# Kernel optimization log

Measured on AMD Instinct MI355X. Metric: run time of the kernel, lower is better.

## Reference

```python
import jax, jax.numpy as jnp
import numpy as np
import math

EPS = 1e-12


def _cmul(ar, ai, br, bi):
    return ar * br - ai * bi, ar * bi + ai * br


def _wilson_seed(x):
    # x: (B, 4, L, L) -> conj of canonical Wilson-line path, (B, L, L) re/im
    ux_r, ux_i, uy_r, uy_i = x[:, 0], x[:, 1], x[:, 2], x[:, 3]
    B, L, _ = ux_r.shape
    dt = x.dtype

    def step(c, u):
        cr, ci = c
        ur, ui = u
        nr, ni = _cmul(cr, ci, ur, ui)
        return (nr, ni), (nr, ni)

    # cumulative complex product along x at y=0
    init_r = jnp.ones((B,), dt)
    init_i = jnp.zeros((B,), dt)
    xs = (ux_r[:, :-1, 0].T, ux_i[:, :-1, 0].T)  # (L-1, B)
    _, (axr, axi) = jax.lax.scan(step, (init_r, init_i), xs)
    x_axis_r = jnp.concatenate([init_r[None], axr], 0).T  # (B, L)
    x_axis_i = jnp.concatenate([init_i[None], axi], 0).T

    # cumulative complex product along y, vectorized over x
    ys = (jnp.moveaxis(uy_r[:, :, :-1], 2, 0), jnp.moveaxis(uy_i[:, :, :-1], 2, 0))  # (L-1, B, L)
    _, (pr, pi_) = jax.lax.scan(step, (x_axis_r, x_axis_i), ys)
    path_r = jnp.moveaxis(jnp.concatenate([x_axis_r[None], pr], 0), 0, 2)  # (B, L, L)
    path_i = jnp.moveaxis(jnp.concatenate([x_axis_i[None], pi_], 0), 0, 2)
    return path_r, -path_i  # conjugate


def _wrap(t):
    return (t + math.pi) % (2.0 * math.pi) - math.pi


def _initial_features(x):
    seed_r, seed_i = _wilson_seed(x)
    ax = jnp.arctan2(x[:, 1], x[:, 0])
    ay = jnp.arctan2(x[:, 3], x[:, 2])
    plaq = _wrap(ax + jnp.roll(ay, -1, axis=1) - jnp.roll(ax, -1, axis=2) - ay)
    pc = jnp.cos(plaq)
    pavg = (pc + jnp.roll(pc, 1, 1) + jnp.roll(pc, -1, 1)
            + jnp.roll(pc, 1, 2) + jnp.roll(pc, -1, 2)) / 5.0
    scalars = jnp.stack([jnp.ones_like(pc), pc, pavg], axis=1)  # (B, 3, L, L)
    return seed_r[:, None] * scalars, seed_i[:, None] * scalars


def _transport_fwd(fr, fi, x, mu):
    lr, li = (x[:, 0], x[:, 1]) if mu == 0 else (x[:, 2], x[:, 3])
    sr = jnp.roll(fr, -1, axis=mu + 2)
    si = jnp.roll(fi, -1, axis=mu + 2)
    return _cmul(lr[:, None], li[:, None], sr, si)


def _transport_bwd(fr, fi, x, mu):
    lr, li = (x[:, 0], x[:, 1]) if mu == 0 else (x[:, 2], x[:, 3])
    cr = jnp.roll(lr, 1, axis=mu + 1)
    ci = jnp.roll(-li, 1, axis=mu + 1)
    sr = jnp.roll(fr, 1, axis=mu + 2)
    si = jnp.roll(fi, 1, axis=mu + 2)
    return _cmul(cr[:, None], ci[:, None], sr, si)


def _lconv(fr, fi, x, center, fwd_w, bwd_w):
    out_r = jnp.einsum('oi,bixy->boxy', center, fr)
    out_i = jnp.einsum('oi,bixy->boxy', center, fi)
    for mu in range(2):
        fr2, fi2 = _transport_fwd(fr, fi, x, mu)
        br2, bi2 = _transport_bwd(fr, fi, x, mu)
        out_r = out_r + jnp.einsum('oi,bixy->boxy', fwd_w[mu], fr2) \
                      + jnp.einsum('oi,bixy->boxy', bwd_w[mu], br2)
        out_i = out_i + jnp.einsum('oi,bixy->boxy', fwd_w[mu], fi2) \
                      + jnp.einsum('oi,bixy->boxy', bwd_w[mu], bi2)
    return out_r, out_i


def _modrelu(fr, fi, bias):
    mag = jnp.sqrt(fr * fr + fi * fi + EPS)
    act = jax.nn.relu(mag + bias[None, :, None, None])
    scale = act / jnp.maximum(mag, EPS)
    return fr * scale, fi * scale


def setup_inputs() -> dict:
    key = jax.random.key(0)
    ks = jax.random.split(key, 11)
    B, L, H, O = 64, 128, 16, 8
    s = 0.1
    return {
        'x': jax.random.normal(ks[0], (B, 4, L, L), jnp.float32),
        'center1': s * jax.random.normal(ks[1], (H, 3), jnp.float32),
        'fwd_w1': s * jax.random.normal(ks[2], (2, H, 3), jnp.float32),
        'bwd_w1': s * jax.random.normal(ks[3], (2, H, 3), jnp.float32),
        'bias1': jnp.zeros((H,), jnp.float32),
        'center2': s * jax.random.normal(ks[4], (O, H), jnp.float32),
        'fwd_w2': s * jax.random.normal(ks[5], (2, O, H), jnp.float32),
        'bwd_w2': s * jax.random.normal(ks[6], (2, O, H), jnp.float32),
        'bias2': jnp.zeros((O,), jnp.float32),
        'ro_weight': s * jax.random.normal(ks[7], (O,), jnp.float32),
        'ro_bias': jnp.zeros((1,), jnp.float32),
    }


def reference(x, center1, fwd_w1, bwd_w1, bias1, center2, fwd_w2, bwd_w2, bias2, ro_weight, ro_bias):
    fr, fi = _initial_features(x)
    fr, fi = _lconv(fr, fi, x, center1, fwd_w1, bwd_w1)
    fr, fi = _modrelu(fr, fi, bias1)
    fr, fi = _lconv(fr, fi, x, center2, fwd_w2, bwd_w2)
    fr, fi = _modrelu(fr, fi, bias2)
    inv = fr * fr + fi * fi
    return jnp.einsum('c,bcxy->bxy', ro_weight, inv)[:, None] + ro_bias.reshape(1, 1, 1, 1)
```

## Files before the change

kernel.cpp:

```cpp
#include <hip/hip_runtime.h>
#include <math.h>

#define LQ   128
#define BQ   64
#define LL   (LQ*LQ)
#define H1   16
#define O2   8
#define TILE 16
#define REG  18
#define NPTS (REG*REG)
#define PCR  22
#define PCN  (PCR*PCR)
#define LKR  23
#define LKN  (LKR*LKR)
#define SDR  20
#define SDN  (SDR*SDR)
#define FSTR 10

typedef float f2 __attribute__((ext_vector_type(2)));
using bf8 = __attribute__((ext_vector_type(8))) short;
using f4  = __attribute__((ext_vector_type(4))) float;

__device__ __forceinline__ int wrapi(int v) { return v & (LQ - 1); }

__device__ __forceinline__ unsigned pack_bf(float hi, float lo) {
    return __builtin_amdgcn_perm(__float_as_uint(hi), __float_as_uint(lo),
                                 0x07060302u);
}
__device__ __forceinline__ unsigned bfrne(float f) {
    unsigned u = __float_as_uint(f);
    u += 0x7fffu + ((u >> 16) & 1u);
    return u >> 16;
}

#define WS_W1 ((size_t)BQ * LL)

__global__ __launch_bounds__(256)
void k_scan(const float* __restrict__ x,
            const float* __restrict__ c1, const float* __restrict__ fw1,
            const float* __restrict__ bw1, float* __restrict__ ws) {
    int blk = blockIdx.x;
    if (blk == BQ * 8) {
        int tid = threadIdx.x;
        if (tid < 120) {
            int t = tid / 24, r = tid - t * 24;
            int c = r >> 3, op = r & 7;
            const float* src = (t == 0) ? c1 : (t == 1) ? fw1 : (t == 2) ? bw1
                             : (t == 3) ? (fw1 + 48) : (bw1 + 48);
            float2 v = make_float2(src[(2 * op) * 3 + c], src[(2 * op + 1) * 3 + c]);
            ((float2*)ws)[WS_W1 + tid] = v;
        }
        return;
    }
    int b = blk >> 3, rq = blk & 7;
    int l = threadIdx.x & 63, w = threadIdx.x >> 6;
    const float* x0 = x + (size_t)b * 4 * LL;
    const float* x1 = x0 + LL;

    float ur0 = x0[(2 * l) * LQ],     ui0 = x1[(2 * l) * LQ];
    float ur1 = x0[(2 * l + 1) * LQ], ui1 = x1[(2 * l + 1) * LQ];
    float pr = ur0 * ur1 - ui0 * ui1;
    float pi = ur0 * ui1 + ui0 * ur1;
    for (int d = 1; d < 64; d <<= 1) {
        float qr = __shfl_up(pr, d, 64);
        float qi = __shfl_up(pi, d, 64);
        if (l >= d) {
            float nr = qr * pr - qi * pi;
            float ni = qr * pi + qi * pr;
            pr = nr; pi = ni;
        }
    }
    float er = __shfl_up(pr, 1, 64);
    float ei = __shfl_up(pi, 1, 64);
    if (l == 0) { er = 1.f; ei = 0.f; }
    float e1r = er * ur0 - ei * ui0;
    float e1i = er * ui0 + ei * ur0;

    const float* yrp = x + (size_t)(b * 4 + 2) * LL;
    const float* yip = yrp + LL;
    float4* seed4 = (float4*)ws;

    for (int k = 0; k < 4; ++k) {
        int i = rq * 16 + w * 4 + k;
        float cxr = __shfl((i & 1) ? e1r : er, i >> 1, 64);
        float cxi = __shfl((i & 1) ? e1i : ei, i >> 1, 64);
        const float* yr = yrp + (size_t)i * LQ;
        const float* yi = yip + (size_t)i * LQ;
        float vr0 = yr[2 * l],     vi0 = yi[2 * l];
        float vr1 = yr[2 * l + 1], vi1 = yi[2 * l + 1];
        float sr = vr0 * vr1 - vi0 * vi1;
        float si = vr0 * vi1 + vi0 * vr1;
        for (int d = 1; d < 64; d <<= 1) {
            float qr = __shfl_up(sr, d, 64);
            float qi = __shfl_up(si, d, 64);
            if (l >= d) {
                float nr = qr * sr - qi * si;
                float ni = qr * si + qi * sr;
                sr = nr; si = ni;
            }
        }
        float gr = __shfl_up(sr, 1, 64);
        float gi = __shfl_up(si, 1, 64);
        if (l == 0) { gr = 1.f; gi = 0.f; }
        float s0r = cxr * gr - cxi * gi;
        float s0i = cxr * gi + cxi * gr;
        float s1r = s0r * vr0 - s0i * vi0;
        float s1i = s0r * vi0 + s0i * vr0;
        seed4[((size_t)b * LL + (size_t)i * LQ) / 2 + l] =
            make_float4(s0r, -s0i, s1r, -s1i);
    }
}

__global__ __launch_bounds__(256, 4)
void k_main(const float* __restrict__ x,
            const float* __restrict__ c2, const float* __restrict__ fw2,
            const float* __restrict__ bw2, const float* __restrict__ b1,
            const float* __restrict__ b2,
            const float* __restrict__ ro, const float* __restrict__ rob,
            const float* __restrict__ ws, float* __restrict__ out) {
    __shared__ unsigned s_f1r[NPTS * FSTR];
    __shared__ unsigned s_f1i[NPTS * FSTR];
    __shared__ f2 s_ux[LKN];
    __shared__ f2 s_uy[LKN];
    __shared__ float s_pc[PCN];
    __shared__ f2 s_sd[SDN];
    int tid = threadIdx.x;
    int b = blockIdx.z, i0 = blockIdx.y * TILE, j0 = blockIdx.x * TILE;
    const float* x0 = x + (size_t)b * 4 * LL;
    const float* x1 = x0 + LL;
    const float* x2 = x0 + 2 * LL;
    const float* x3 = x0 + 3 * LL;
    const float2* seed = (const float2*)ws + (size_t)b * LL;
    const float2* W1 = (const float2*)ws + WS_W1;

    bool z1 = true;
#pragma unroll
    for (int h = 0; h < H1; ++h) z1 = z1 && (b1[h] == 0.f);
    bool z2 = true;
#pragma unroll
    for (int o = 0; o < O2; ++o) z2 = z2 && (b2[o] == 0.f);

    for (int p = tid; p < LKN; p += 256) {
        int ri = p / LKR, rj = p - ri * LKR;
        int gi = wrapi(i0 - 3 + ri), gj = wrapi(j0 - 3 + rj);
        int idx = gi * LQ + gj;
        s_ux[p] = (f2){x0[idx], x1[idx]};
        s_uy[p] = (f2){x2[idx], x3[idx]};
    }
    for (int p = tid; p < SDN; p += 256) {
        int ri = p / SDR, rj = p - ri * SDR;
        int gi = wrapi(i0 - 2 + ri), gj = wrapi(j0 - 2 + rj);
        float2 s = seed[gi * LQ + gj];
        s_sd[p] = (f2){s.x, s.y};
    }
    __syncthreads();

    for (int p = tid; p < PCN; p += 256) {
        int ri = p / PCR, rj = p - ri * PCR;
        int lb = ri * LKR + rj;
        f2 u1 = s_ux[lb];
        f2 u2 = s_uy[lb + LKR];
        f2 u3 = s_ux[lb + 1];
        f2 u4 = s_uy[lb];
        float ar = u1.x * u2.x - u1.y * u2.y, ai = u1.x * u2.y + u1.y * u2.x;
        float br = ar * u3.x + ai * u3.y,     bi = -ar * u3.y + ai * u3.x;
        float zr = br * u4.x + bi * u4.y,     zi = -br * u4.y + bi * u4.x;
        s_pc[p] = zr * __frsqrt_rn(fmaf(zr, zr, zi * zi) + 1e-30f);
    }
    __syncthreads();

#pragma unroll
    for (int pass = 0; pass < 2; ++pass) {
        int p = tid + pass * 256;
        if (pass == 1 && p >= NPTS) break;
        int ri = p / REG, rj = p - ri * REG;
        int sc = (ri + 1) * SDR + (rj + 1);
        int lb = (ri + 2) * LKR + (rj + 2);
        int cb = (ri + 2) * PCR + (rj + 2);

        f2 t[5]; float tc[5], tv[5];
        {
            f2 SC = s_sd[sc], SXP = s_sd[sc + SDR], SXM = s_sd[sc - SDR];
            f2 SYP = s_sd[sc + 1], SYM = s_sd[sc - 1];
            f2 lx = s_ux[lb], ly = s_uy[lb];
            f2 mx = s_ux[lb - LKR], my = s_uy[lb - 1];
            t[0] = SC;
            t[1] = (f2){lx.x * SXP.x - lx.y * SXP.y, lx.x * SXP.y + lx.y * SXP.x};
            t[2] = (f2){mx.x * SXM.x + mx.y * SXM.y, mx.x * SXM.y - mx.y * SXM.x};
            t[3] = (f2){ly.x * SYP.x - ly.y * SYP.y, ly.x * SYP.y + ly.y * SYP.x};
            t[4] = (f2){my.x * SYM.x + my.y * SYM.y, my.x * SYM.y - my.y * SYM.x};
            float p00 = s_pc[cb];
            float pP0 = s_pc[cb + PCR],     pM0 = s_pc[cb - PCR];
            float p0P = s_pc[cb + 1],       p0M = s_pc[cb - 1];
            float pP20 = s_pc[cb + 2*PCR],  pM20 = s_pc[cb - 2*PCR];
            float p0P2 = s_pc[cb + 2],      p0M2 = s_pc[cb - 2];
            float pPP = s_pc[cb + PCR + 1], pPM = s_pc[cb + PCR - 1];
            float pMP = s_pc[cb - PCR + 1], pMM = s_pc[cb - PCR - 1];
            tc[0] = p00; tc[1] = pP0; tc[2] = pM0; tc[3] = p0P; tc[4] = p0M;
            tv[0] = (p00 + pP0 + pM0 + p0P + p0M) * 0.2f;
            tv[1] = (pP0 + pP20 + p00 + pPP + pPM) * 0.2f;
            tv[2] = (pM0 + p00 + pM20 + pMP + pMM) * 0.2f;
            tv[3] = (p0P + pPP + pMP + p0P2 + p00) * 0.2f;
            tv[4] = (p0M + pPM + pMM + p00 + p0M2) * 0.2f;
        }

        f2 accr[8], acci[8];
#pragma unroll
        for (int op = 0; op < 8; ++op) { accr[op] = (f2){0.f, 0.f}; acci[op] = (f2){0.f, 0.f}; }
#pragma unroll
        for (int q = 0; q < 5; ++q) {
            f2 tcv = (f2){tc[q], tc[q]}, tvv = (f2){tv[q], tv[q]};
            f2 trv = (f2){t[q].x, t[q].x}, tiv = (f2){t[q].y, t[q].y};
            const float2* Wq = W1 + q * 24;
#pragma unroll
            for (int op = 0; op < 8; ++op) {
                float2 w0 = Wq[op], w1 = Wq[8 + op], w2 = Wq[16 + op];
                f2 mp = (f2){w0.x, w0.y};
                mp += (f2){w1.x, w1.y} * tcv;
                mp += (f2){w2.x, w2.y} * tvv;
                accr[op] += mp * trv;
                acci[op] += mp * tiv;
            }
        }
        if (!z1) {
#pragma unroll
            for (int op = 0; op < 8; ++op) {
                f2 q2 = accr[op] * accr[op] + acci[op] * acci[op] + (f2){1e-12f, 1e-12f};
                float s0 = fmaxf(fmaf(b1[2 * op],     __frsqrt_rn(q2.x), 1.f), 0.f);
                float s1 = fmaxf(fmaf(b1[2 * op + 1], __frsqrt_rn(q2.y), 1.f), 0.f);
                f2 sv = (f2){s0, s1};
                accr[op] *= sv; acci[op] *= sv;
            }
        }
        unsigned* fr_ = &s_f1r[p * FSTR];
        unsigned* fi_ = &s_f1i[p * FSTR];
#pragma unroll
        for (int d = 0; d < 4; ++d) {
            unsigned r0 = pack_bf(accr[2*d].y,   accr[2*d].x);
            unsigned r1 = pack_bf(accr[2*d+1].y, accr[2*d+1].x);
            unsigned q0 = pack_bf(acci[2*d].y,   acci[2*d].x);
            unsigned q1 = pack_bf(acci[2*d+1].y, acci[2*d+1].x);
            *(uint2*)&fr_[2*d] = make_uint2(r0, r1);
            *(uint2*)&fi_[2*d] = make_uint2(q0, q1);
        }
    }
    __syncthreads();

    int lane = tid & 63, w = tid >> 6;
    int quad = lane >> 4, nIdx = lane & 15;
    int half = quad >> 1;
    int koff = (quad & 1) * 4;

    const float* wLo[3] = {c2, bw2, bw2 + O2 * H1};
    const float* wHi[3] = {fw2, fw2 + O2 * H1, (const float*)0};
    bf8 afr[3];
#pragma unroll
    for (int pq = 0; pq < 3; ++pq) {
        bf8 z = {0, 0, 0, 0, 0, 0, 0, 0};
        const float* wsrc = half ? wHi[pq] : wLo[pq];
        int row = half ? (nIdx - 8) : nIdx;
        bool valid = half ? (nIdx >= 8 && wsrc != 0) : (nIdx < 8);
        if (valid) {
            const float* wp = wsrc + row * H1 + (quad & 1) * 8;
            float4 wa = *(const float4*)wp;
            float4 wb = *(const float4*)(wp + 4);
            uint4 u;
            u.x = bfrne(wa.x) | (bfrne(wa.y) << 16);
            u.y = bfrne(wa.z) | (bfrne(wa.w) << 16);
            u.z = bfrne(wb.x) | (bfrne(wb.y) << 16);
            u.w = bfrne(wb.z) | (bfrne(wb.w) << 16);
            __builtin_memcpy(&z, &u, 16);
        }
        afr[pq] = z;
    }
    float4 ro_lo = *(const float4*)ro;
    float4 ro_hi = *(const float4*)(ro + 4);
    float4 b2_lo = *(const float4*)b2;
    float4 b2_hi = *(const float4*)(b2 + 4);
    float4 zf4 = make_float4(0.f, 0.f, 0.f, 0.f);
    float4 rv = (quad == 0) ? ro_lo : ((quad == 1) ? ro_hi : zf4);
    float4 bv = (quad == 0) ? b2_lo : ((quad == 1) ? b2_hi : zf4);
    float rob0 = rob[0];

    for (int g = 0; g < 4; ++g) {
        int row = w * 4 + g;
        int posc = (row + 1) * REG + (nIdx + 1);
        int lb2 = (row + 3) * LKR + (nIdx + 3);
        f2 lx = s_ux[lb2], ly = s_uy[lb2];
        f2 mx = s_ux[lb2 - LKR], my = s_uy[lb2 - 1];

        float Lr[3], Li[3];
        Lr[0] = half ? lx.x : 1.f;   Li[0] = half ? lx.y : 0.f;
        Lr[1] = half ? ly.x : mx.x;  Li[1] = half ? ly.y : -mx.y;
        Lr[2] = half ? 0.f : my.x;   Li[2] = half ? 0.f : -my.y;
        int dpl[3];
        dpl[0] = half ? REG : 0;
        dpl[1] = half ? 1 : -REG;
        dpl[2] = -1;

        f4 a2r = {0.f, 0.f, 0.f, 0.f}, a2i = {0.f, 0.f, 0.f, 0.f};
#pragma unroll
        for (int pq = 0; pq < 3; ++pq) {
            int base = (posc + dpl[pq]) * FSTR + koff;
            uint2 rlo = *(const uint2*)&s_f1r[base];
            uint2 rhi = *(const uint2*)&s_f1r[base + 2];
            uint2 ilo = *(const uint2*)&s_f1i[base];
            uint2 ihi = *(const uint2*)&s_f1i[base + 2];
            bf8 br, bi;
            uint4 ur = {rlo.x, rlo.y, rhi.x, rhi.y};
            uint4 ui = {ilo.x, ilo.y, ihi.x, ihi.y};
            __builtin_memcpy(&br, &ur, 16);
            __builtin_memcpy(&bi, &ui, 16);
            f4 zc = {0.f, 0.f, 0.f, 0.f};
            f4 sr = __builtin_amdgcn_mfma_f32_16x16x32_bf16(afr[pq], br, zc, 0, 0, 0);
            f4 si = __builtin_amdgcn_mfma_f32_16x16x32_bf16(afr[pq], bi, zc, 0, 0, 0);
            a2r += Lr[pq] * sr - Li[pq] * si;
            a2i += Lr[pq] * si + Li[pq] * sr;
        }

#pragma unroll
        for (int c = 0; c < 4; ++c) {
            a2r[c] += __shfl_xor(a2r[c], 32, 64);
            a2i[c] += __shfl_xor(a2i[c], 32, 64);
        }

        f4 q4 = a2r * a2r + a2i * a2i;
        float res;
        if (z2) {
            res = rv.x * q4.x + rv.y * q4.y + rv.z * q4.z + rv.w * q4.w;
        } else {
            float bvv[4] = {bv.x, bv.y, bv.z, bv.w};
            float rvv[4] = {rv.x, rv.y, rv.z, rv.w};
            res = 0.f;
#pragma unroll
            for (int r = 0; r < 4; ++r) {
                float qq = q4[r];
                float s = fmaxf(fmaf(bvv[r], __frsqrt_rn(qq + 1e-12f), 1.f), 0.f);
                res = fmaf(rvv[r], s * s * qq, res);
            }
        }
        res += __shfl_xor(res, 16, 64);
        if (quad == 0)
            out[(size_t)b * LL + (size_t)(i0 + row) * LQ + (j0 + nIdx)] = res + rob0;
    }
}

extern "C" void kernel_launch(void* const* d_in, const int* in_sizes, int n_in,
                              void* d_out, int out_size, void* d_ws, size_t ws_size,
                              hipStream_t stream) {
    const float* x   = (const float*)d_in[0];
    const float* c1  = (const float*)d_in[1];
    const float* fw1 = (const float*)d_in[2];
    const float* bw1 = (const float*)d_in[3];
    const float* b1  = (const float*)d_in[4];
    const float* c2  = (const float*)d_in[5];
    const float* fw2 = (const float*)d_in[6];
    const float* bw2 = (const float*)d_in[7];
    const float* b2  = (const float*)d_in[8];
    const float* ro  = (const float*)d_in[9];
    const float* rob = (const float*)d_in[10];
    float* out = (float*)d_out;
    float* ws  = (float*)d_ws;

    k_scan<<<BQ * 8 + 1, 256, 0, stream>>>(x, c1, fw1, bw1, ws);
    dim3 grid(LQ / TILE, LQ / TILE, BQ);
    k_main<<<grid, 256, 0, stream>>>(x, c2, fw2, bw2, b1, b2,
                                     ro, rob, ws, out);
}
```

Before: 136.3 us.

## Shrink LDS footprint with dense uint4 feature layout and bf16 seed tile

The intermediate layer-1 feature tiles move from a padded stride-10 unsigned layout to a dense uint4 layout, so each point is written and read with 128-bit LDS accesses instead of pairs of 64-bit ones. The seed halo tile is stored as packed bf16 pairs rather than float2, halving its shared memory. Launch bounds are raised to 5 blocks per CU to use the smaller LDS footprint for occupancy. The risks are extra bank conflicts from dropping the padding, added register pressure under the tighter bound, and slightly lower seed precision.

```diff
diff --git a/kernel.cpp b/kernel.cpp
--- a/kernel.cpp
+++ b/kernel.cpp
@@ -15,7 +15,6 @@
 #define LKN  (LKR*LKR)
 #define SDR  20
 #define SDN  (SDR*SDR)
-#define FSTR 10
 
 typedef float f2 __attribute__((ext_vector_type(2)));
 using bf8 = __attribute__((ext_vector_type(8))) short;
@@ -111,19 +110,19 @@
     }
 }
 
-__global__ __launch_bounds__(256, 4)
+__global__ __launch_bounds__(256, 5)
 void k_main(const float* __restrict__ x,
             const float* __restrict__ c2, const float* __restrict__ fw2,
             const float* __restrict__ bw2, const float* __restrict__ b1,
             const float* __restrict__ b2,
             const float* __restrict__ ro, const float* __restrict__ rob,
             const float* __restrict__ ws, float* __restrict__ out) {
-    __shared__ unsigned s_f1r[NPTS * FSTR];
-    __shared__ unsigned s_f1i[NPTS * FSTR];
+    __shared__ uint4 s_f1r4[NPTS * 2];
+    __shared__ uint4 s_f1i4[NPTS * 2];
     __shared__ f2 s_ux[LKN];
     __shared__ f2 s_uy[LKN];
     __shared__ float s_pc[PCN];
-    __shared__ f2 s_sd[SDN];
+    __shared__ unsigned s_sd[SDN];
     int tid = threadIdx.x;
     int b = blockIdx.z, i0 = blockIdx.y * TILE, j0 = blockIdx.x * TILE;
     const float* x0 = x + (size_t)b * 4 * LL;
@@ -151,7 +150,7 @@
         int ri = p / SDR, rj = p - ri * SDR;
         int gi = wrapi(i0 - 2 + ri), gj = wrapi(j0 - 2 + rj);
         float2 s = seed[gi * LQ + gj];
-        s_sd[p] = (f2){s.x, s.y};
+        s_sd[p] = bfrne(s.x) | (bfrne(s.y) << 16);
     }
     __syncthreads();
 
@@ -180,8 +179,13 @@
 
         f2 t[5]; float tc[5], tv[5];
         {
-            f2 SC = s_sd[sc], SXP = s_sd[sc + SDR], SXM = s_sd[sc - SDR];
-            f2 SYP = s_sd[sc + 1], SYM = s_sd[sc - 1];
+            unsigned uC  = s_sd[sc],     uXP = s_sd[sc + SDR];
+            unsigned uXM = s_sd[sc - SDR], uYP = s_sd[sc + 1], uYM = s_sd[sc - 1];
+            f2 SC  = (f2){__uint_as_float(uC  << 16), __uint_as_float(uC  & 0xffff0000u)};
+            f2 SXP = (f2){__uint_as_float(uXP << 16), __uint_as_float(uXP & 0xffff0000u)};
+            f2 SXM = (f2){__uint_as_float(uXM << 16), __uint_as_float(uXM & 0xffff0000u)};
+            f2 SYP = (f2){__uint_as_float(uYP << 16), __uint_as_float(uYP & 0xffff0000u)};
+            f2 SYM = (f2){__uint_as_float(uYM << 16), __uint_as_float(uYM & 0xffff0000u)};
             f2 lx = s_ux[lb], ly = s_uy[lb];
             f2 mx = s_ux[lb - LKR], my = s_uy[lb - 1];
             t[0] = SC;
@@ -232,24 +236,24 @@
                 accr[op] *= sv; acci[op] *= sv;
             }
         }
-        unsigned* fr_ = &s_f1r[p * FSTR];
-        unsigned* fi_ = &s_f1i[p * FSTR];
-#pragma unroll
-        for (int d = 0; d < 4; ++d) {
-            unsigned r0 = pack_bf(accr[2*d].y,   accr[2*d].x);
-            unsigned r1 = pack_bf(accr[2*d+1].y, accr[2*d+1].x);
-            unsigned q0 = pack_bf(acci[2*d].y,   acci[2*d].x);
-            unsigned q1 = pack_bf(acci[2*d+1].y, acci[2*d+1].x);
-            *(uint2*)&fr_[2*d] = make_uint2(r0, r1);
-            *(uint2*)&fi_[2*d] = make_uint2(q0, q1);
-        }
+        uint4 ra, rb, ia, ib;
+        ra.x = pack_bf(accr[0].y, accr[0].x); ra.y = pack_bf(accr[1].y, accr[1].x);
+        ra.z = pack_bf(accr[2].y, accr[2].x); ra.w = pack_bf(accr[3].y, accr[3].x);
+        rb.x = pack_bf(accr[4].y, accr[4].x); rb.y = pack_bf(accr[5].y, accr[5].x);
+        rb.z = pack_bf(accr[6].y, accr[6].x); rb.w = pack_bf(accr[7].y, accr[7].x);
+        ia.x = pack_bf(acci[0].y, acci[0].x); ia.y = pack_bf(acci[1].y, acci[1].x);
+        ia.z = pack_bf(acci[2].y, acci[2].x); ia.w = pack_bf(acci[3].y, acci[3].x);
+        ib.x = pack_bf(acci[4].y, acci[4].x); ib.y = pack_bf(acci[5].y, acci[5].x);
+        ib.z = pack_bf(acci[6].y, acci[6].x); ib.w = pack_bf(acci[7].y, acci[7].x);
+        s_f1r4[p * 2] = ra; s_f1r4[p * 2 + 1] = rb;
+        s_f1i4[p * 2] = ia; s_f1i4[p * 2 + 1] = ib;
     }
     __syncthreads();
 
     int lane = tid & 63, w = tid >> 6;
     int quad = lane >> 4, nIdx = lane & 15;
     int half = quad >> 1;
-    int koff = (quad & 1) * 4;
+    int ksel = quad & 1;
 
     const float* wLo[3] = {c2, bw2, bw2 + O2 * H1};
     const float* wHi[3] = {fw2, fw2 + O2 * H1, (const float*)0};
@@ -261,7 +265,7 @@
         int row = half ? (nIdx - 8) : nIdx;
         bool valid = half ? (nIdx >= 8 && wsrc != 0) : (nIdx < 8);
         if (valid) {
-            const float* wp = wsrc + row * H1 + (quad & 1) * 8;
+            const float* wp = wsrc + row * H1 + ksel * 8;
             float4 wa = *(const float4*)wp;
             float4 wb = *(const float4*)(wp + 4);
             uint4 u;
@@ -301,14 +305,10 @@
         f4 a2r = {0.f, 0.f, 0.f, 0.f}, a2i = {0.f, 0.f, 0.f, 0.f};
 #pragma unroll
         for (int pq = 0; pq < 3; ++pq) {
-            int base = (posc + dpl[pq]) * FSTR + koff;
-            uint2 rlo = *(const uint2*)&s_f1r[base];
-            uint2 rhi = *(const uint2*)&s_f1r[base + 2];
-            uint2 ilo = *(const uint2*)&s_f1i[base];
-            uint2 ihi = *(const uint2*)&s_f1i[base + 2];
+            int bidx = (posc + dpl[pq]) * 2 + ksel;
+            uint4 ur = s_f1r4[bidx];
+            uint4 ui = s_f1i4[bidx];
             bf8 br, bi;
-            uint4 ur = {rlo.x, rlo.y, rhi.x, rhi.y};
-            uint4 ui = {ilo.x, ilo.y, ihi.x, ihi.y};
             __builtin_memcpy(&br, &ur, 16);
             __builtin_memcpy(&bi, &ui, 16);
             f4 zc = {0.f, 0.f, 0.f, 0.f};
```

New measurement: 135.6 us. Within noise of the previous version (-0.5%).
